# Kernel optimization log

Hardware: AMD Instinct MI355X
Metric: run time of the kernel (lower is better)

The kernel has to match this reference:

```python
import jax, jax.numpy as jnp
import numpy as np

N_S = 50000
N_T = 50000
E = 800000
D_IN = 128
D_OUT = 128


def setup_inputs() -> dict:
    key = jax.random.key(0)
    k1, k2, k3, k4 = jax.random.split(key, 4)
    edge_index = jax.random.randint(k1, (2, E), 0, N_S, dtype=jnp.int64)
    x_s = jax.random.normal(k2, (N_S, D_IN), dtype=jnp.float32)
    x_t = jax.random.normal(k3, (N_T, D_IN), dtype=jnp.float32)
    # glorot-ish linear weight of GCNConv (bias=False)
    W = jax.random.normal(k4, (D_IN, D_OUT), dtype=jnp.float32) * (1.0 / np.sqrt(D_IN))
    return {"edge_index": edge_index, "x_s": x_s, "x_t": x_t, "W": W}


def reference(edge_index, x_s, x_t, W):
    N_s = x_s.shape[0]
    N_t = x_t.shape[0]
    N = N_s + N_t
    # dropout p=0.0 -> identity; concat bipartite features
    x = jnp.concatenate([x_s, x_t], axis=0)  # [N, d_in]
    row = edge_index[0]
    col = edge_index[1] + N_s  # module shifts target indices in-place
    # GCNConv: add self-loops with weight 1
    loops = jnp.arange(N, dtype=row.dtype)
    row_f = jnp.concatenate([row, loops])
    col_f = jnp.concatenate([col, loops])
    w = jnp.ones(row_f.shape[0], dtype=x.dtype)
    # symmetric degree normalization: deg computed on target (col)
    deg = jax.ops.segment_sum(w, col_f, num_segments=N)
    deg_inv_sqrt = jnp.where(deg > 0, jax.lax.rsqrt(deg), 0.0)
    norm = deg_inv_sqrt[row_f] * deg_inv_sqrt[col_f]  # [E+N]
    # linear transform then normalized scatter-add aggregation
    h = x @ W  # [N, d_out]
    msg = h[row_f] * norm[:, None]  # gather + scale, [E+N, d_out]
    out = jax.ops.segment_sum(msg, col_f, num_segments=N)  # scatter-add
    out = jax.nn.relu(out)
    return out[:N_s], out[N_s:]
```

## Files before the change

### kernel.cpp

```cpp
#include <hip/hip_runtime.h>
#include <hip/hip_bf16.h>
#include <math.h>

#define NSRC 50000
#define NTGT 50000
#define NTOT 100000
#define NEDGE 800000
#define DIM 128

#define NBUCK 782
#define BCAP 1536
#define BPAD 16
#define BLK 512
#define EPT 16
#define EPB 8192
#define PBLK 98
#define GEMM_GRID 782
#define FGRID (PBLK + GEMM_GRID)

typedef __attribute__((ext_vector_type(8))) short short8;
typedef __attribute__((ext_vector_type(4))) float float4v;

union U8 { short8 s; uint4 u; };

__device__ __forceinline__ unsigned short f2bf(float f) {
    unsigned u = __float_as_uint(f);
    unsigned r = (u + 0x7FFFu + ((u >> 16) & 1u)) >> 16;
    return (unsigned short)r;
}
__device__ __forceinline__ float bf2f(unsigned us) {
    return __uint_as_float(us << 16);
}
__device__ __forceinline__ unsigned pkbf(float lo, float hi) {
    __hip_bfloat162 b = __float22bfloat162_rn(make_float2(lo, hi));
    return *(unsigned*)&b;
}

__global__ __launch_bounds__(256) void k_prep(const float* __restrict__ W,
                                              unsigned short* __restrict__ Wt,
                                              int* __restrict__ bcnt) {
    int i = blockIdx.x * 256 + threadIdx.x;
    if (i < NBUCK * BPAD) bcnt[i] = 0;
    int j = i & 7, lane = (i >> 3) & 63, ts = i >> 9;
    int t = ts >> 2, s = ts & 3;
    int nl = lane & 15, qd = lane >> 4;
    Wt[i] = f2bf(W[(s * 32 + qd * 8 + j) * DIM + (t * 16 + nl)]);
}

__global__ __launch_bounds__(BLK) void k_front(const int* __restrict__ row,
                                               const int* __restrict__ col,
                                               int* __restrict__ bcnt,
                                               unsigned* __restrict__ part,
                                               const float* __restrict__ xsrc,
                                               const float* __restrict__ xtgt,
                                               const unsigned short* __restrict__ Wt,
                                               unsigned short* __restrict__ h,
                                               float* __restrict__ out) {
    __shared__ union SM {
        struct { int hist[NBUCK]; int runbase[NBUCK]; int cur[NBUCK]; } p;
        unsigned short Bs[DIM * DIM];
    } sm;

    const int tid = threadIdx.x;
    const int bid = blockIdx.x;

    if (bid < PBLK) {
        for (int i = tid; i < NBUCK; i += BLK) sm.p.hist[i] = 0;
        __syncthreads();

        int e0 = bid * EPB + tid * EPT;
        bool valid = (e0 + EPT <= NEDGE);
        int c[EPT], r[EPT];
        if (valid) {
#pragma unroll
            for (int v = 0; v < 4; ++v) {
                *(int4*)&c[4 * v] = *(const int4*)(col + e0 + 4 * v);
                *(int4*)&r[4 * v] = *(const int4*)(row + e0 + 4 * v);
            }
#pragma unroll
            for (int i = 0; i < EPT; ++i) atomicAdd(&sm.p.hist[c[i] >> 6], 1);
        }
        __syncthreads();
        for (int i = tid; i < NBUCK; i += BLK) {
            sm.p.runbase[i] = atomicAdd(&bcnt[i * BPAD], sm.p.hist[i]);
            sm.p.cur[i] = 0;
        }
        __syncthreads();
        if (valid) {
#pragma unroll
            for (int i = 0; i < EPT; ++i) {
                int q = c[i] >> 6;
                int pos = sm.p.runbase[q] + atomicAdd(&sm.p.cur[q], 1);
                part[q * BCAP + pos] = (unsigned)r[i] | ((unsigned)(c[i] & 63) << 16);
            }
        }
        return;
    }

    const int gb = bid - PBLK;

    for (int idx = tid; idx < 2048; idx += BLK)
        ((uint4*)sm.Bs)[idx] = ((const uint4*)Wt)[idx];

    const int wave = tid >> 6, lane = tid & 63;
    const int nl = lane & 15, quad = lane >> 4;

    int node = gb * 128 + wave * 16 + nl;
    int mc = (node < NTOT) ? node : (NTOT - 1);
    const float* xrow = (mc < NSRC) ? (xsrc + (size_t)mc * DIM)
                                    : (xtgt + (size_t)(mc - NSRC) * DIM);
    float4 a[8];
#pragma unroll
    for (int s = 0; s < 4; ++s) {
        a[2 * s]     = *(const float4*)(xrow + s * 32 + quad * 8);
        a[2 * s + 1] = *(const float4*)(xrow + s * 32 + quad * 8 + 4);
    }
    __syncthreads();

    float4v acc[8];
#pragma unroll
    for (int t = 0; t < 8; ++t) acc[t] = (float4v){0.f, 0.f, 0.f, 0.f};

#pragma unroll
    for (int s = 0; s < 4; ++s) {
        U8 af;
        af.u.x = pkbf(a[2 * s].x, a[2 * s].y);
        af.u.y = pkbf(a[2 * s].z, a[2 * s].w);
        af.u.z = pkbf(a[2 * s + 1].x, a[2 * s + 1].y);
        af.u.w = pkbf(a[2 * s + 1].z, a[2 * s + 1].w);
#pragma unroll
        for (int t = 0; t < 8; ++t) {
            short8 bf = *(const short8*)&sm.Bs[((t * 4 + s) * 64 + lane) * 8];
            acc[t] = __builtin_amdgcn_mfma_f32_16x16x32_bf16(bf, af.s, acc[t], 0, 0, 0);
        }
    }

    if (node < NTOT) {
        unsigned short* hp = h + (size_t)node * DIM + quad * 4;
        float* op = out + (size_t)node * DIM + quad * 4;
        bool isrc = (node < NSRC);
#pragma unroll
        for (int t = 0; t < 8; ++t) {
            uint2 p;
            p.x = pkbf(acc[t][0], acc[t][1]);
            p.y = pkbf(acc[t][2], acc[t][3]);
            *(uint2*)(hp + t * 16) = p;
            if (isrc) {
                float4 o;
                o.x = fmaxf(acc[t][0], 0.f);
                o.y = fmaxf(acc[t][1], 0.f);
                o.z = fmaxf(acc[t][2], 0.f);
                o.w = fmaxf(acc[t][3], 0.f);
                *(float4*)(op + t * 16) = o;
            }
        }
    }
}

__global__ __launch_bounds__(BLK) void k_back(const int* __restrict__ bcnt,
                                              const unsigned* __restrict__ part,
                                              const unsigned short* __restrict__ h,
                                              float* __restrict__ out) {
    __shared__ unsigned ebuf[BCAP];
    __shared__ unsigned short srt[BCAP];
    __shared__ int hist[64], bufA[64], bufB[64], cur[64], st[64];

    int q = blockIdx.x, tid = threadIdx.x;
    int n = bcnt[q * BPAD];
    int base = q * BCAP;

    if (tid < 64) hist[tid] = 0;
    __syncthreads();
    for (int i = tid; i < n; i += BLK) {
        unsigned p = part[base + i];
        ebuf[i] = p;
        atomicAdd(&hist[p >> 16], 1);
    }
    __syncthreads();

    if (tid < 64) bufA[tid] = hist[tid];
    int* src = bufA; int* dst = bufB;
    for (int d = 1; d < 64; d <<= 1) {
        __syncthreads();
        if (tid < 64) dst[tid] = src[tid] + ((tid >= d) ? src[tid - d] : 0);
        int* tp = src; src = dst; dst = tp;
    }
    __syncthreads();
    if (tid < 64) {
        int excl = src[tid] - hist[tid];
        cur[tid] = excl;
        st[tid] = excl;
    }
    __syncthreads();
    for (int i = tid; i < n; i += BLK) {
        unsigned p = ebuf[i];
        int pos = atomicAdd(&cur[p >> 16], 1);
        srt[pos] = (unsigned short)(p & 0xffffu);
    }
    __syncthreads();

    int w = tid >> 6, lane = tid & 63;
    int qd = lane >> 4, ql = lane & 15;
    int cl0 = w * 8;

#define GATHER(ACC, NN, SS)                                                   \
    if (e < NN) {                                                             \
        int r = (int)srt[SS + e];                                             \
        uint4 d = *(const uint4*)(h + (size_t)r * DIM + ql * 8);              \
        ACC[0] += bf2f(d.x & 0xffff); ACC[1] += bf2f(d.x >> 16);              \
        ACC[2] += bf2f(d.y & 0xffff); ACC[3] += bf2f(d.y >> 16);              \
        ACC[4] += bf2f(d.z & 0xffff); ACC[5] += bf2f(d.z >> 16);              \
        ACC[6] += bf2f(d.w & 0xffff); ACC[7] += bf2f(d.w >> 16);              \
    }

#define WRITEOUT(ACC, NN, CL)                                                 \
    {                                                                         \
        _Pragma("unroll")                                                     \
        for (int i = 0; i < 8; ++i) {                                         \
            ACC[i] += __shfl_xor(ACC[i], 16, 64);                             \
            ACC[i] += __shfl_xor(ACC[i], 32, 64);                             \
        }                                                                     \
        int cgl = q * 64 + (CL);                                              \
        if (qd == 0 && cgl < NTGT) {                                          \
            float di = rsqrtf(1.0f + (float)NN);                              \
            float dd = di * di;                                               \
            uint4 dh = *(const uint4*)(h + (size_t)(NSRC + cgl) * DIM + ql * 8); \
            float4 o0, o1;                                                    \
            o0.x = fmaxf(di * ACC[0] + dd * bf2f(dh.x & 0xffff), 0.f);        \
            o0.y = fmaxf(di * ACC[1] + dd * bf2f(dh.x >> 16), 0.f);           \
            o0.z = fmaxf(di * ACC[2] + dd * bf2f(dh.y & 0xffff), 0.f);        \
            o0.w = fmaxf(di * ACC[3] + dd * bf2f(dh.y >> 16), 0.f);           \
            o1.x = fmaxf(di * ACC[4] + dd * bf2f(dh.z & 0xffff), 0.f);        \
            o1.y = fmaxf(di * ACC[5] + dd * bf2f(dh.z >> 16), 0.f);           \
            o1.z = fmaxf(di * ACC[6] + dd * bf2f(dh.w & 0xffff), 0.f);        \
            o1.w = fmaxf(di * ACC[7] + dd * bf2f(dh.w >> 16), 0.f);           \
            float* op = out + (size_t)(NSRC + cgl) * DIM + ql * 8;            \
            *(float4*)op = o0;                                                \
            *(float4*)(op + 4) = o1;                                          \
        }                                                                     \
    }

    for (int g = 0; g < 2; ++g) {
        int c0 = cl0 + g * 4;
        int nA = hist[c0],     sA = st[c0];
        int nB = hist[c0 + 1], sB = st[c0 + 1];
        int nC = hist[c0 + 2], sC = st[c0 + 2];
        int nD = hist[c0 + 3], sD = st[c0 + 3];

        float accA[8], accB[8], accC[8], accD[8];
#pragma unroll
        for (int i = 0; i < 8; ++i) {
            accA[i] = 0.f; accB[i] = 0.f; accC[i] = 0.f; accD[i] = 0.f;
        }

        int m1 = (nA > nB) ? nA : nB;
        int m2 = (nC > nD) ? nC : nD;
        int mx = (m1 > m2) ? m1 : m2;
        int itn = (mx + 3) >> 2;
        for (int k = 0; k < itn; ++k) {
            int e = 4 * k + qd;
            GATHER(accA, nA, sA)
            GATHER(accB, nB, sB)
            GATHER(accC, nC, sC)
            GATHER(accD, nD, sD)
        }

        WRITEOUT(accA, nA, c0)
        WRITEOUT(accB, nB, c0 + 1)
        WRITEOUT(accC, nC, c0 + 2)
        WRITEOUT(accD, nD, c0 + 3)
    }
#undef GATHER
#undef WRITEOUT
}

extern "C" void kernel_launch(void* const* d_in, const int* in_sizes, int n_in,
                              void* d_out, int out_size, void* d_ws, size_t ws_size,
                              hipStream_t stream) {
    const int* ei     = (const int*)d_in[0];
    const float* xsrc = (const float*)d_in[1];
    const float* xtgt = (const float*)d_in[2];
    const float* W    = (const float*)d_in[3];
    float* out = (float*)d_out;

    const int* row = ei;
    const int* col = ei + NEDGE;

    char* ws = (char*)d_ws;
    unsigned short* h  = (unsigned short*)ws;  ws += (size_t)NTOT * DIM * 2;
    unsigned short* Wt = (unsigned short*)ws;  ws += DIM * DIM * 2;
    unsigned* part = (unsigned*)ws;            ws += (size_t)NBUCK * BCAP * 4;
    int* bcnt = (int*)ws;                      ws += NBUCK * BPAD * 4;

    k_prep<<<64, 256, 0, stream>>>(W, Wt, bcnt);
    k_front<<<FGRID, BLK, 0, stream>>>(row, col, bcnt, part, xsrc, xtgt, Wt, h, out);
    k_back<<<NBUCK, BLK, 0, stream>>>(bcnt, part, h, out);
}
```

Measured before the change: 158.8 us.

## Stage bucketed edges in shared memory to coalesce partition writes

The partition blocks now sort their edges into shared memory by bucket, using a Hillis-Steele prefix scan over bucket counts. They then write the packed edges to global memory in contiguous, coalesced runs instead of scattered per-edge stores. The edges per block are halved and the partition block count doubled to fit the new shared-memory staging arrays and spread the work. The cost is ten scan passes with barriers and extra shared-memory traffic per block, in exchange for fewer uncoalesced global writes.

```diff
diff --git a/kernel.cpp b/kernel.cpp
--- a/kernel.cpp
+++ b/kernel.cpp
@@ -12,9 +12,9 @@
 #define BCAP 1536
 #define BPAD 16
 #define BLK 512
-#define EPT 16
-#define EPB 8192
-#define PBLK 98
+#define EPT 8
+#define EPB 4096
+#define PBLK 196
 #define GEMM_GRID 782
 #define FGRID (PBLK + GEMM_GRID)
 
@@ -57,7 +57,14 @@
                                                unsigned short* __restrict__ h,
                                                float* __restrict__ out) {
     __shared__ union SM {
-        struct { int hist[NBUCK]; int runbase[NBUCK]; int cur[NBUCK]; } p;
+        struct {
+            int scanA[1024];
+            int scanB[1024];
+            int cur[NBUCK];
+            int off[NBUCK];
+            unsigned srt[EPB];
+            unsigned short sb[EPB];
+        } p;
         unsigned short Bs[DIM * DIM];
     } sm;
 
@@ -65,34 +72,55 @@
     const int bid = blockIdx.x;
 
     if (bid < PBLK) {
-        for (int i = tid; i < NBUCK; i += BLK) sm.p.hist[i] = 0;
+        int n = NEDGE - bid * EPB; if (n > EPB) n = EPB;
+
+        for (int i = tid; i < 1024; i += BLK) sm.p.scanA[i] = 0;
         __syncthreads();
 
         int e0 = bid * EPB + tid * EPT;
         bool valid = (e0 + EPT <= NEDGE);
         int c[EPT], r[EPT];
         if (valid) {
-#pragma unroll
-            for (int v = 0; v < 4; ++v) {
-                *(int4*)&c[4 * v] = *(const int4*)(col + e0 + 4 * v);
-                *(int4*)&r[4 * v] = *(const int4*)(row + e0 + 4 * v);
-            }
-#pragma unroll
-            for (int i = 0; i < EPT; ++i) atomicAdd(&sm.p.hist[c[i] >> 6], 1);
-        }
-        __syncthreads();
-        for (int i = tid; i < NBUCK; i += BLK) {
-            sm.p.runbase[i] = atomicAdd(&bcnt[i * BPAD], sm.p.hist[i]);
-            sm.p.cur[i] = 0;
-        }
-        __syncthreads();
+            *(int4*)&c[0] = *(const int4*)(col + e0);
+            *(int4*)&c[4] = *(const int4*)(col + e0 + 4);
+            *(int4*)&r[0] = *(const int4*)(row + e0);
+            *(int4*)&r[4] = *(const int4*)(row + e0 + 4);
+#pragma unroll
+            for (int i = 0; i < EPT; ++i) atomicAdd(&sm.p.scanA[c[i] >> 6], 1);
+        }
+        __syncthreads();
+
+        int* src = sm.p.scanA; int* dst = sm.p.scanB;
+        for (int d = 1; d < 1024; d <<= 1) {
+            for (int i = tid; i < 1024; i += BLK)
+                dst[i] = src[i] + ((i >= d) ? src[i - d] : 0);
+            __syncthreads();
+            int* tp = src; src = dst; dst = tp;
+        }
+        for (int q = tid; q < NBUCK; q += BLK) {
+            int incl = src[q];
+            int excl = (q > 0) ? src[q - 1] : 0;
+            int cnt = incl - excl;
+            sm.p.cur[q] = excl;
+            int rb = cnt ? atomicAdd(&bcnt[q * BPAD], cnt) : 0;
+            sm.p.off[q] = q * BCAP + rb - excl;
+        }
+        __syncthreads();
+
         if (valid) {
 #pragma unroll
             for (int i = 0; i < EPT; ++i) {
                 int q = c[i] >> 6;
-                int pos = sm.p.runbase[q] + atomicAdd(&sm.p.cur[q], 1);
-                part[q * BCAP + pos] = (unsigned)r[i] | ((unsigned)(c[i] & 63) << 16);
+                int pos = atomicAdd(&sm.p.cur[q], 1);
+                sm.p.srt[pos] = (unsigned)r[i] | ((unsigned)(c[i] & 63) << 16);
+                sm.p.sb[pos] = (unsigned short)q;
             }
+        }
+        __syncthreads();
+
+        for (int j = tid; j < n; j += BLK) {
+            int q = sm.p.sb[j];
+            part[sm.p.off[q] + j] = sm.p.srt[j];
         }
         return;
     }
```

Result: slower. 164.7 us (+3.7%).
